# Kernel tuning notes

Hardware: AMD Instinct MI355X
Metric: run time of the kernel (lower is better)

## Reference

```python
import jax, jax.numpy as jnp
import numpy as np

B, L, D, NH, K, R = 2, 1024, 768, 12, 24, 768
HD = D // NH            # head_dim = 64
NFFT = 2048             # nearest power of two >= 2*L-1


def _spectral_filters():
    # Hankel matrix Z_{ij} = 2 / ((i+j)^3 - (i+j)), top-K eigvecs scaled by sigma^{1/4}
    e = np.arange(1, L + 1, dtype=np.float64)
    ipj = e[:, None] + e[None, :]
    Z = 2.0 / (ipj ** 3 - ipj)
    sigma, phi = np.linalg.eigh(Z)
    phi_k = phi[:, -K:] * (sigma[-K:] ** 0.25)
    return jnp.asarray(phi_k, dtype=jnp.float32)  # (L, K)


def setup_inputs() -> dict:
    key = jax.random.key(0)
    ks = jax.random.split(key, 16)
    s = 0.02
    lin = lambda k_, i, o: jax.random.normal(k_, (i, o), jnp.float32) * s
    return {
        "x": jax.random.normal(ks[0], (B, L, D), jnp.float32),
        "stu_filters": _spectral_filters(),
        "M_inputs": jax.random.normal(ks[1], (D, R), jnp.float32) * s,
        "M_filters": jax.random.normal(ks[2], (K, R), jnp.float32) * s,
        "wq_w": lin(ks[3], D, D), "wq_b": jnp.zeros((D,), jnp.float32),
        "wk_w": lin(ks[4], D, D), "wk_b": jnp.zeros((D,), jnp.float32),
        "wv_w": lin(ks[5], D, D), "wv_b": jnp.zeros((D,), jnp.float32),
        "wg_w": lin(ks[6], D, D), "wg_b": jnp.zeros((D,), jnp.float32),
        "wo_w": lin(ks[7], D, D), "wo_b": jnp.zeros((D,), jnp.float32),
    }


def _stu_features(x, stu_filters, M_inputs, M_filters):
    # tensordot STU path: project inputs and filters to rank R, then FFT causal conv
    u = x @ M_inputs                       # (B, L, R)
    phi = stu_filters @ M_filters          # (L, R)
    sgn = jnp.where(jnp.arange(L) % 2 == 0, 1.0, -1.0)[None, :, None]  # (1, L, 1)
    V = jnp.fft.rfft(phi, n=NFFT, axis=0)  # (NFFT//2+1, R)
    U = jnp.stack([u, u * sgn], axis=-1)   # (B, L, R, 2)
    Uf = jnp.fft.rfft(U, n=NFFT, axis=1)   # (B, NFFT//2+1, R, 2)
    conv = jnp.fft.irfft(V[None, :, :, None] * Uf, n=NFFT, axis=1)[:, :L]  # (B, L, R, 2)
    u_plus = conv[..., 0]
    u_minus = conv[..., 1] * sgn
    return u_plus + u_minus               # (B, L, R) with R == D


def reference(x, stu_filters, M_inputs, M_filters,
              wq_w, wq_b, wk_w, wk_b, wv_w, wv_b,
              wg_w, wg_b, wo_w, wo_b):
    x_tilde = _stu_features(x, stu_filters, M_inputs, M_filters)  # (B, L, D)

    heads = lambda y: y.reshape(B, L, NH, HD).transpose(0, 2, 1, 3)  # (B, H, L, h)
    q = heads(x @ wq_w + wq_b)
    k = heads(x @ wk_w + wk_b)
    v = heads(x @ wv_w + wv_b)

    # causal linear attention via cumulative outer-product state
    Z = jnp.einsum('bhtp,bhtn->bhtpn', v, k)     # (B, H, L, h, h)
    Hc = jnp.cumsum(Z, axis=2)
    Y = jnp.einsum('bhtp,bhtpn->bhtn', q, Hc)    # (B, H, L, h)
    y_attn = Y.transpose(0, 2, 1, 3).reshape(B, L, D)

    gate = jax.nn.sigmoid(x @ wg_w + wg_b)
    y = x_tilde + (y_attn - x_tilde) * gate
    return y @ wo_w + wo_b
```

## Files before the change

### kernel.cpp

```cpp
#include <hip/hip_runtime.h>
#include <math.h>

#define B_  2
#define L_  1024
#define D_  768
#define NH_ 12
#define HD_ 64
#define K_  24
#define R_  768
#define NC_ 16
#define CS_ 64

typedef __bf16 bf16x8 __attribute__((ext_vector_type(8)));
typedef float f32x4 __attribute__((ext_vector_type(4)));
typedef float f32x8 __attribute__((ext_vector_type(8)));
typedef unsigned short u16x8 __attribute__((ext_vector_type(8)));

__device__ inline unsigned short f2bf(float f) {
    union { float f; unsigned u; } v; v.f = f;
    unsigned r = v.u + 0x7FFFu + ((v.u >> 16) & 1u);
    return (unsigned short)(r >> 16);
}

__device__ inline ushort4 pack4(const f32x4 v) {
    ushort4 r;
    r.x = f2bf(v[0]); r.y = f2bf(v[1]); r.z = f2bf(v[2]); r.w = f2bf(v[3]);
    return r;
}

__device__ inline u16x8 pack8(const f32x8 v) {
    u16x8 r;
#pragma unroll
    for (int e = 0; e < 8; ++e) r[e] = f2bf(v[e]);
    return r;
}

__device__ inline f32x8 bf2f8(const u16x8 v) {
    f32x8 r;
#pragma unroll
    for (int e = 0; e < 8; ++e) {
        union { float f; unsigned u; } t;
        t.u = ((unsigned)v[e]) << 16;
        r[e] = t.f;
    }
    return r;
}

#define GLD_LDS16(g, l)                                                     \
    __builtin_amdgcn_global_load_lds(                                       \
        (const __attribute__((address_space(1))) void*)(g),                 \
        (__attribute__((address_space(3))) void*)(l), 16, 0, 0)

__global__ __launch_bounds__(256) void k_prep(const float* __restrict__ w0,
                                              const float* __restrict__ w1,
                                              const float* __restrict__ w2,
                                              const float* __restrict__ w3,
                                              const float* __restrict__ w4,
                                              const float* __restrict__ w5,
                                              unsigned short* __restrict__ Wt,
                                              const float* __restrict__ x,
                                              unsigned short* __restrict__ xb) {
    const int bid = blockIdx.x;
    const int tid = threadIdx.x;
    if (bid < 864) {
        const int z = bid / 144, rem = bid % 144;
        const float* W;
        switch (z) {
            case 0: W = w0; break;
            case 1: W = w1; break;
            case 2: W = w2; break;
            case 3: W = w3; break;
            case 4: W = w4; break;
            default: W = w5; break;
        }
        unsigned short* o = Wt + (size_t)z * D_ * D_;
        __shared__ float t[64][69];
        const int n0 = (rem % 12) * 64, k0 = (rem / 12) * 64;
        const int row = tid >> 4, c4 = (tid & 15) * 4;
#pragma unroll
        for (int i = 0; i < 4; ++i) {
            const float4 v = *reinterpret_cast<const float4*>(
                W + (size_t)(k0 + row + i * 16) * D_ + n0 + c4);
            t[row + i * 16][c4 + 0] = v.x;
            t[row + i * 16][c4 + 1] = v.y;
            t[row + i * 16][c4 + 2] = v.z;
            t[row + i * 16][c4 + 3] = v.w;
        }
        __syncthreads();
        const int orow = tid >> 4, oc4 = (tid & 15) * 4;
#pragma unroll
        for (int i = 0; i < 4; ++i) {
            const int nn = orow + i * 16;
            ushort4 o4;
            o4.x = f2bf(t[oc4 + 0][nn]);
            o4.y = f2bf(t[oc4 + 1][nn]);
            o4.z = f2bf(t[oc4 + 2][nn]);
            o4.w = f2bf(t[oc4 + 3][nn]);
            *reinterpret_cast<ushort4*>(o + (size_t)(n0 + nn) * D_ + k0 + oc4) = o4;
        }
    } else {
        const int i8 = ((bid - 864) * 256 + tid) * 8;
        float4 f0 = *reinterpret_cast<const float4*>(x + i8);
        float4 f1 = *reinterpret_cast<const float4*>(x + i8 + 4);
        u16x8 p;
        p[0] = f2bf(f0.x); p[1] = f2bf(f0.y); p[2] = f2bf(f0.z); p[3] = f2bf(f0.w);
        p[4] = f2bf(f1.x); p[5] = f2bf(f1.y); p[6] = f2bf(f1.z); p[7] = f2bf(f1.w);
        *reinterpret_cast<u16x8*>(xb + i8) = p;
    }
}

template <int FM, int FN>
__device__ __forceinline__ void gemm_core(const unsigned short* __restrict__ A,
                                          const unsigned short* __restrict__ Bt,
                                          const float* __restrict__ bias,
                                          int mode,
                                          float* __restrict__ cf,
                                          unsigned short* __restrict__ cbf,
                                          unsigned short* __restrict__ ct,
                                          int N, int Kd,
                                          int bm, int bn, int tid) {
    constexpr int BM = 2 * FM * 16;
    constexpr int BN = 2 * FN * 16;
    constexpr int CTS = BM + 4;
    __shared__ unsigned short smem[2 * BM * 64 + 2 * BN * 64];
    unsigned short (*As)[BM * 64] = (unsigned short (*)[BM * 64])smem;
    unsigned short (*Bs)[BN * 64] = (unsigned short (*)[BN * 64])(smem + 2 * BM * 64);
    const int lane = tid & 63, wave = tid >> 6;
    const int wm = (wave >> 1) * (FM * 16), wn = (wave & 1) * (FN * 16);
    const int l15 = lane & 15, lg = lane >> 4;

    f32x4 acc[FM][FN] = {};

    auto stage = [&](int buf, int k0) {
#pragma unroll
        for (int q = 0; q < FM; ++q) {
            const int s = q * 256 + tid;
            GLD_LDS16(A + (size_t)(bm + (s >> 3)) * Kd + k0 + (s & 7) * 8,
                      &As[buf][s * 8]);
        }
#pragma unroll
        for (int q = 0; q < FN; ++q) {
            const int s = q * 256 + tid;
            GLD_LDS16(Bt + (size_t)(bn + (s >> 3)) * Kd + k0 + (s & 7) * 8,
                      &Bs[buf][s * 8]);
        }
    };

    stage(0, 0);
    __syncthreads();
    int cur = 0;
    const int nt = Kd / 64;
    for (int t = 0; t < nt; ++t) {
        if (t + 1 < nt) stage(cur ^ 1, (t + 1) * 64);
#pragma unroll
        for (int ks = 0; ks < 2; ++ks) {
            const int kb = ks * 32 + lg * 8;
            bf16x8 a[FM], b[FN];
#pragma unroll
            for (int f = 0; f < FM; ++f)
                a[f] = *reinterpret_cast<const bf16x8*>(
                    &As[cur][(wm + f * 16 + l15) * 64 + kb]);
#pragma unroll
            for (int f = 0; f < FN; ++f)
                b[f] = *reinterpret_cast<const bf16x8*>(
                    &Bs[cur][(wn + f * 16 + l15) * 64 + kb]);
#pragma unroll
            for (int fm = 0; fm < FM; ++fm)
#pragma unroll
                for (int fn = 0; fn < FN; ++fn)
                    acc[fm][fn] = __builtin_amdgcn_mfma_f32_16x16x32_bf16(
                        a[fm], b[fn], acc[fm][fn], 0, 0, 0);
        }
        __syncthreads();
        cur ^= 1;
    }

#pragma unroll
    for (int fm = 0; fm < FM; ++fm)
#pragma unroll
        for (int fn = 0; fn < FN; ++fn) {
            const int cl = wn + fn * 16 + l15;
            const int col = bn + cl;
            const float bv = bias ? bias[col] : 0.f;
            const int rl = wm + fm * 16 + lg * 4;
            const int r0 = bm + rl;
            f32x4 v = acc[fm][fn];
            v[0] += bv; v[1] += bv; v[2] += bv; v[3] += bv;
            if (mode == 0) {
#pragma unroll
                for (int j = 0; j < 4; ++j)
                    cf[(size_t)(r0 + j) * N + col] = v[j];
            }
            if (mode & 1) {
#pragma unroll
                for (int j = 0; j < 4; ++j)
                    cbf[(size_t)(r0 + j) * D_ + col] = f2bf(v[j]);
            }
            if (mode & 2) {
                *reinterpret_cast<ushort4*>(&smem[cl * CTS + rl]) = pack4(v);
            }
        }

    if (mode & 2) {
        __syncthreads();
        const int bI = bm >> 10, l0 = bm & 1023;
#pragma unroll
        for (int q = 0; q < BN * BM / 8 / 256; ++q) {
            const int slot = q * 256 + tid;
            const int cl = slot / (BM / 8), seg = slot % (BM / 8);
            const int gcol = bn + cl;
            const int h = gcol >> 6, n = gcol & 63;
            *reinterpret_cast<u16x8*>(
                ct + (((size_t)bI * NH_ + h) * 64 + n) * (size_t)L_ + l0 + seg * 8) =
                *reinterpret_cast<const u16x8*>(&smem[cl * CTS + seg * 8]);
        }
    }
}

__global__ __launch_bounds__(256) void k_gemm(const unsigned short* __restrict__ A,
                                              const unsigned short* __restrict__ Bt,
                                              const float* __restrict__ bias,
                                              float* __restrict__ C,
                                              int N, int Kd) {
    gemm_core<1, 2>(A, Bt, bias, 0, C, nullptr, nullptr, N, Kd,
                    blockIdx.y * 32, blockIdx.x * 64, threadIdx.x);
}

__global__ __launch_bounds__(256) void k_gemm5(const unsigned short* __restrict__ A,
                                               const unsigned short* __restrict__ wt,
                                               const float* __restrict__ bq,
                                               const float* __restrict__ bk,
                                               const float* __restrict__ bv,
                                               const float* __restrict__ bg,
                                               unsigned short* __restrict__ ubf,
                                               unsigned short* __restrict__ qbf,
                                               unsigned short* __restrict__ ktb,
                                               unsigned short* __restrict__ vbf,
                                               unsigned short* __restrict__ vtb,
                                               unsigned short* __restrict__ gbf) {
    const int z = blockIdx.z;
    const float* bias = nullptr;
    int mode = 1;
    unsigned short* cbf = nullptr; unsigned short* ct = nullptr;
    switch (z) {
        case 0: mode = 1; cbf = ubf; bias = nullptr; break;
        case 1: mode = 1; cbf = qbf; bias = bq; break;
        case 2: mode = 2; ct = ktb; bias = bk; break;
        case 3: mode = 3; cbf = vbf; ct = vtb; bias = bv; break;
        default: mode = 1; cbf = gbf; bias = bg; break;
    }
    const unsigned short* Bt = wt + (size_t)z * D_ * D_;
    gemm_core<4, 4>(A, Bt, bias, mode, nullptr, cbf, ct, D_, D_,
                    blockIdx.y * 128, blockIdx.x * 128, threadIdx.x);
}

__global__ __launch_bounds__(256) void k_attn(const unsigned short* __restrict__ qbf,
                                              const unsigned short* __restrict__ vbf,
                                              const unsigned short* __restrict__ ktb,
                                              const unsigned short* __restrict__ vtb,
                                              unsigned short* __restrict__ yab,
                                              const float* __restrict__ F,
                                              const float* __restrict__ Mf,
                                              unsigned short* __restrict__ phiev) {
    const int tid = threadIdx.x;
    if (blockIdx.x >= 384) {
        const int idx = ((int)blockIdx.x - 384) * 256 + tid;
        const int r = idx % R_;
        const int n = idx / R_;
        float acc = 0.f;
#pragma unroll
        for (int kk = 0; kk < K_; ++kk)
            acc += F[(2 * n) * K_ + kk] * Mf[kk * R_ + r];
        phiev[idx] = f2bf(2.f * acc);
        return;
    }
    const int c = blockIdx.x & 15, h = (blockIdx.x >> 4) % NH_, b = blockIdx.x / (16 * NH_);
    __shared__ unsigned short Qs[64 * 64];
    __shared__ unsigned short Vs[64 * 64];
    __shared__ unsigned short Kc[64 * 64];
    __shared__ unsigned short Tk[2][64 * 64];
    __shared__ unsigned short Tv[2][64 * 64];
    __shared__ unsigned short Sl[64 * 72];
    __shared__ unsigned short Hl[64 * 72];

    const int lane = tid & 63, wave = tid >> 6;
    const int wr = (wave >> 1) * 32, wc = (wave & 1) * 32;
    const int l15 = lane & 15, lg = lane >> 4;

    {
        const size_t rowbase = ((size_t)(b * L_ + c * CS_)) * D_ + h * HD_;
        const size_t tbase = ((size_t)(b * NH_ + h)) * 64 * (size_t)L_ + c * 64;
#pragma unroll
        for (int q2 = 0; q2 < 2; ++q2) {
            const int s = q2 * 256 + tid;
            const int row = s >> 3, c8 = s & 7;
            GLD_LDS16(qbf + rowbase + (size_t)row * D_ + c8 * 8, &Qs[s * 8]);
            GLD_LDS16(vbf + rowbase + (size_t)row * D_ + c8 * 8, &Vs[s * 8]);
            GLD_LDS16(ktb + tbase + (size_t)row * L_ + c8 * 8, &Kc[s * 8]);
        }
    }

    auto stage_t = [&](int buf, int cc) {
        const size_t tb2 = ((size_t)(b * NH_ + h)) * 64 * (size_t)L_ + cc * 64;
#pragma unroll
        for (int q2 = 0; q2 < 2; ++q2) {
            const int s = q2 * 256 + tid;
            const int row = s >> 3, c8 = s & 7;
            GLD_LDS16(ktb + tb2 + (size_t)row * L_ + c8 * 8, &Tk[buf][s * 8]);
            GLD_LDS16(vtb + tb2 + (size_t)row * L_ + c8 * 8, &Tv[buf][s * 8]);
        }
    };

    if (c > 0) stage_t(0, 0);
    __syncthreads();

    f32x4 hacc[2][2] = {};
    int cur = 0;
    for (int cc = 0; cc < c; ++cc) {
        if (cc + 1 < c) stage_t(cur ^ 1, cc + 1);
#pragma unroll
        for (int ks = 0; ks < 2; ++ks) {
            const int kb = ks * 32 + lg * 8;
            bf16x8 av[2], bk[2];
#pragma unroll
            for (int f = 0; f < 2; ++f) {
                av[f] = *reinterpret_cast<const bf16x8*>(&Tv[cur][(wr + f * 16 + l15) * 64 + kb]);
                bk[f] = *reinterpret_cast<const bf16x8*>(&Tk[cur][(wc + f * 16 + l15) * 64 + kb]);
            }
#pragma unroll
            for (int fm = 0; fm < 2; ++fm)
#pragma unroll
                for (int fn = 0; fn < 2; ++fn)
                    hacc[fm][fn] = __builtin_amdgcn_mfma_f32_16x16x32_bf16(
                        av[fm], bk[fn], hacc[fm][fn], 0, 0, 0);
        }
        __syncthreads();
        cur ^= 1;
    }

    if (c > 0) {
#pragma unroll
        for (int fm = 0; fm < 2; ++fm)
#pragma unroll
            for (int fn = 0; fn < 2; ++fn) {
                const int n = wc + fn * 16 + l15;
                const int p0 = wr + fm * 16 + lg * 4;
                *reinterpret_cast<ushort4*>(&Hl[n * 72 + p0]) = pack4(hacc[fm][fn]);
            }
    }

    {
        f32x4 sacc[2][2] = {};
#pragma unroll
        for (int ks = 0; ks < 2; ++ks) {
            const int kb = ks * 32 + lg * 8;
            bf16x8 av[2], bq[2];
#pragma unroll
            for (int f = 0; f < 2; ++f) {
                av[f] = *reinterpret_cast<const bf16x8*>(&Vs[(wr + f * 16 + l15) * 64 + kb]);
                bq[f] = *reinterpret_cast<const bf16x8*>(&Qs[(wc + f * 16 + l15) * 64 + kb]);
            }
#pragma unroll
            for (int fm = 0; fm < 2; ++fm)
#pragma unroll
                for (int fn = 0; fn < 2; ++fn)
                    sacc[fm][fn] = __builtin_amdgcn_mfma_f32_16x16x32_bf16(
                        av[fm], bq[fn], sacc[fm][fn], 0, 0, 0);
        }
#pragma unroll
        for (int fm = 0; fm < 2; ++fm)
#pragma unroll
            for (int fn = 0; fn < 2; ++fn) {
                const int t = wc + fn * 16 + l15;
                const int s0 = wr + fm * 16 + lg * 4;
#pragma unroll
                for (int j = 0; j < 4; ++j)
                    if (s0 + j > t) sacc[fm][fn][j] = 0.f;
                *reinterpret_cast<ushort4*>(&Sl[t * 72 + s0]) = pack4(sacc[fm][fn]);
            }
    }
    __syncthreads();

    f32x4 yacc[2][2] = {};
#pragma unroll
    for (int ks = 0; ks < 2; ++ks) {
        const int kb = ks * 32 + lg * 8;
        bf16x8 ak[2], bs[2];
#pragma unroll
        for (int f = 0; f < 2; ++f) {
            ak[f] = *reinterpret_cast<const bf16x8*>(&Kc[(wr + f * 16 + l15) * 64 + kb]);
            bs[f] = *reinterpret_cast<const bf16x8*>(&Sl[(wc + f * 16 + l15) * 72 + kb]);
        }
#pragma unroll
        for (int fm = 0; fm < 2; ++fm)
#pragma unroll
            for (int fn = 0; fn < 2; ++fn)
                yacc[fm][fn] = __builtin_amdgcn_mfma_f32_16x16x32_bf16(
                    ak[fm], bs[fn], yacc[fm][fn], 0, 0, 0);
    }
    if (c > 0) {
#pragma unroll
        for (int ks = 0; ks < 2; ++ks) {
            const int kb = ks * 32 + lg * 8;
            bf16x8 ah[2], bq[2];
#pragma unroll
            for (int f = 0; f < 2; ++f) {
                ah[f] = *reinterpret_cast<const bf16x8*>(&Hl[(wr + f * 16 + l15) * 72 + kb]);
                bq[f] = *reinterpret_cast<const bf16x8*>(&Qs[(wc + f * 16 + l15) * 64 + kb]);
            }
#pragma unroll
            for (int fm = 0; fm < 2; ++fm)
#pragma unroll
                for (int fn = 0; fn < 2; ++fn)
                    yacc[fm][fn] = __builtin_amdgcn_mfma_f32_16x16x32_bf16(
                        ah[fm], bq[fn], yacc[fm][fn], 0, 0, 0);
        }
    }

#pragma unroll
    for (int fm = 0; fm < 2; ++fm)
#pragma unroll
        for (int fn = 0; fn < 2; ++fn) {
            const int n0 = wr + fm * 16 + lg * 4;
            const int t = wc + fn * 16 + l15;
            const size_t idx = ((size_t)(b * L_ + c * CS_ + t)) * D_ + h * HD_ + n0;
            *reinterpret_cast<ushort4*>(yab + idx) = pack4(yacc[fm][fn]);
        }
}

__global__ __launch_bounds__(768) void k_conv(const unsigned short* __restrict__ ubf,
                                              const unsigned short* __restrict__ phiev,
                                              const unsigned short* __restrict__ yab,
                                              const unsigned short* __restrict__ gbf,
                                              unsigned short* __restrict__ gx) {
    __shared__ u16x8 red[8][8][96];
    const int tid = threadIdx.x;
    const int g   = tid / 96;
    const int lr  = tid % 96;
    const int r   = lr * 8;
    const int m0  = blockIdx.x * 8;
    const int bp  = blockIdx.y;
    const int b   = bp >> 1, p = bp & 1;

    f32x8 acc[8] = {};
    f32x8 w[8]   = {};

    const int ns = g * 64;
    const int ne = min(ns + 64, m0 + 8);

    if (ns < ne) {
        if (g > 0) {
#pragma unroll
            for (int j = 1; j <= 7; ++j)
                w[(8 - j) & 7] = bf2f8(
                    *reinterpret_cast<const u16x8*>(phiev + (size_t)(ns - j) * R_ + r));
        }
        const unsigned short* pp = phiev + (size_t)ns * R_ + r;
        const unsigned short* up =
            ubf + ((size_t)(b * L_) + (size_t)(2 * (m0 + 7 - ns) + p)) * R_ + r;
        for (int i = ns; i < ne; i += 8) {
#pragma unroll
            for (int k = 0; k < 8; ++k) {
                const u16x8 pv = *reinterpret_cast<const u16x8*>(pp);
                const u16x8 uv = *reinterpret_cast<const u16x8*>(up);
                w[k] = bf2f8(pv);
                const f32x8 fu = bf2f8(uv);
#pragma unroll
                for (int a = 0; a < 8; ++a)
                    acc[a] += w[(k + a + 1) & 7] * fu;
                pp += R_;
                up -= 2 * R_;
            }
        }
    }

#pragma unroll
    for (int a = 0; a < 8; ++a) red[g][a][lr] = pack8(acc[a]);
    __syncthreads();

    const int a2 = tid / 96, l2 = tid % 96;
    f32x8 s = {};
#pragma unroll
    for (int g2 = 0; g2 < 8; ++g2) s += bf2f8(red[g2][a2][l2]);

    const size_t idx = ((size_t)(b * L_) + (size_t)(2 * (m0 + a2) + p)) * R_ + l2 * 8;
    const f32x8 yf = bf2f8(*reinterpret_cast<const u16x8*>(yab + idx));
    const f32x8 gf = bf2f8(*reinterpret_cast<const u16x8*>(gbf + idx));
    u16x8 o;
#pragma unroll
    for (int e = 0; e < 8; ++e) {
        const float sg = 1.f / (1.f + expf(-gf[e]));
        o[e] = f2bf(s[e] + (yf[e] - s[e]) * sg);
    }
    *reinterpret_cast<u16x8*>(gx + idx) = o;
}

extern "C" void kernel_launch(void* const* d_in, const int* in_sizes, int n_in,
                              void* d_out, int out_size, void* d_ws, size_t ws_size,
                              hipStream_t stream) {
    const float* x    = (const float*)d_in[0];
    const float* stu  = (const float*)d_in[1];
    const float* Mi   = (const float*)d_in[2];
    const float* Mf   = (const float*)d_in[3];
    const float* wq_w = (const float*)d_in[4];
    const float* wq_b = (const float*)d_in[5];
    const float* wk_w = (const float*)d_in[6];
    const float* wk_b = (const float*)d_in[7];
    const float* wv_w = (const float*)d_in[8];
    const float* wv_b = (const float*)d_in[9];
    const float* wg_w = (const float*)d_in[10];
    const float* wg_b = (const float*)d_in[11];
    const float* wo_w = (const float*)d_in[12];
    const float* wo_b = (const float*)d_in[13];
    float* out = (float*)d_out;

    char* ws = (char*)d_ws;
    size_t o = 0;
    const size_t WSZ = (size_t)D_ * D_;
    unsigned short* wbf   = (unsigned short*)(ws + o); o += 6 * WSZ * 2;
    unsigned short* xbf   = (unsigned short*)(ws + o); o += (size_t)B_ * L_ * D_ * 2;
    unsigned short* gx    = (unsigned short*)(ws + o); o += (size_t)B_ * L_ * D_ * 2;
    unsigned short* qbf   = (unsigned short*)(ws + o); o += (size_t)B_ * L_ * D_ * 2;
    unsigned short* vbf   = (unsigned short*)(ws + o); o += (size_t)B_ * L_ * D_ * 2;
    unsigned short* ubf   = (unsigned short*)(ws + o); o += (size_t)B_ * L_ * D_ * 2;
    unsigned short* gbf   = (unsigned short*)(ws + o); o += (size_t)B_ * L_ * D_ * 2;
    unsigned short* yab   = (unsigned short*)(ws + o); o += (size_t)B_ * L_ * D_ * 2;
    unsigned short* ktb   = (unsigned short*)(ws + o); o += (size_t)B_ * NH_ * 64 * L_ * 2;
    unsigned short* vtb   = (unsigned short*)(ws + o); o += (size_t)B_ * NH_ * 64 * L_ * 2;
    unsigned short* phiev = (unsigned short*)(ws + o); o += (size_t)(L_ / 2) * R_ * 2;

    unsigned short* wo_t = wbf + 5 * WSZ;

    const dim3 blk(256);

    k_prep<<<dim3(1632), blk, 0, stream>>>(Mi, wq_w, wk_w, wv_w, wg_w, wo_w, wbf,
                                           x, xbf);

    k_gemm5<<<dim3(D_ / 128, (B_ * L_) / 128, 5), blk, 0, stream>>>(
        xbf, wbf, wq_b, wk_b, wv_b, wg_b, ubf, qbf, ktb, vbf, vtb, gbf);

    k_attn<<<dim3(384 + 1536), blk, 0, stream>>>(qbf, vbf, ktb, vtb, yab,
                                                 stu, Mf, phiev);

    k_conv<<<dim3(L_ / 2 / 8, B_ * 2), dim3(768), 0, stream>>>(ubf, phiev, yab, gbf, gx);

    k_gemm<<<dim3(D_ / 64, (B_ * L_) / 32), blk, 0, stream>>>(gx, wo_t, wo_b, out, D_, D_);
}
```

Baseline: 91.94 us.

## Fuse five kernels into one persistent kernel with grid barriers

Replaces the five kernel launches (prep, fused QKVG GEMM, attention plus filter projection, convolution, output GEMM) with a single persistent kernel of 512 blocks. Stages are separated by atomic-counter grid barriers, and shared memory is one shared buffer carved up per stage. The conv stage is restructured to use 192 threads with 256-step chunks, and the output GEMM tile changes to 64x64. The aim is to remove launch gaps and tail effects between kernels. In exchange it risks deadlock if all 512 blocks are not co-resident, and it reduces parallelism within stages such as the conv and the final GEMM.

```diff
diff --git a/kernel.cpp b/kernel.cpp
--- a/kernel.cpp
+++ b/kernel.cpp
@@ -51,62 +51,18 @@
         (const __attribute__((address_space(1))) void*)(g),                 \
         (__attribute__((address_space(3))) void*)(l), 16, 0, 0)
 
-__global__ __launch_bounds__(256) void k_prep(const float* __restrict__ w0,
-                                              const float* __restrict__ w1,
-                                              const float* __restrict__ w2,
-                                              const float* __restrict__ w3,
-                                              const float* __restrict__ w4,
-                                              const float* __restrict__ w5,
-                                              unsigned short* __restrict__ Wt,
-                                              const float* __restrict__ x,
-                                              unsigned short* __restrict__ xb) {
-    const int bid = blockIdx.x;
-    const int tid = threadIdx.x;
-    if (bid < 864) {
-        const int z = bid / 144, rem = bid % 144;
-        const float* W;
-        switch (z) {
-            case 0: W = w0; break;
-            case 1: W = w1; break;
-            case 2: W = w2; break;
-            case 3: W = w3; break;
-            case 4: W = w4; break;
-            default: W = w5; break;
-        }
-        unsigned short* o = Wt + (size_t)z * D_ * D_;
-        __shared__ float t[64][69];
-        const int n0 = (rem % 12) * 64, k0 = (rem / 12) * 64;
-        const int row = tid >> 4, c4 = (tid & 15) * 4;
-#pragma unroll
-        for (int i = 0; i < 4; ++i) {
-            const float4 v = *reinterpret_cast<const float4*>(
-                W + (size_t)(k0 + row + i * 16) * D_ + n0 + c4);
-            t[row + i * 16][c4 + 0] = v.x;
-            t[row + i * 16][c4 + 1] = v.y;
-            t[row + i * 16][c4 + 2] = v.z;
-            t[row + i * 16][c4 + 3] = v.w;
-        }
-        __syncthreads();
-        const int orow = tid >> 4, oc4 = (tid & 15) * 4;
-#pragma unroll
-        for (int i = 0; i < 4; ++i) {
-            const int nn = orow + i * 16;
-            ushort4 o4;
-            o4.x = f2bf(t[oc4 + 0][nn]);
-            o4.y = f2bf(t[oc4 + 1][nn]);
-            o4.z = f2bf(t[oc4 + 2][nn]);
-            o4.w = f2bf(t[oc4 + 3][nn]);
-            *reinterpret_cast<ushort4*>(o + (size_t)(n0 + nn) * D_ + k0 + oc4) = o4;
-        }
-    } else {
-        const int i8 = ((bid - 864) * 256 + tid) * 8;
-        float4 f0 = *reinterpret_cast<const float4*>(x + i8);
-        float4 f1 = *reinterpret_cast<const float4*>(x + i8 + 4);
-        u16x8 p;
-        p[0] = f2bf(f0.x); p[1] = f2bf(f0.y); p[2] = f2bf(f0.z); p[3] = f2bf(f0.w);
-        p[4] = f2bf(f1.x); p[5] = f2bf(f1.y); p[6] = f2bf(f1.z); p[7] = f2bf(f1.w);
-        *reinterpret_cast<u16x8*>(xb + i8) = p;
-    }
+#define NBLK 512u
+
+__device__ inline void gridbar(unsigned* cnt) {
+    __syncthreads();
+    if (threadIdx.x == 0) {
+        __threadfence();
+        atomicAdd(cnt, 1u);
+        while (__hip_atomic_load(cnt, __ATOMIC_RELAXED,
+                                 __HIP_MEMORY_SCOPE_AGENT) < NBLK) {}
+        __threadfence();
+    }
+    __syncthreads();
 }
 
 template <int FM, int FN>
@@ -118,13 +74,15 @@
                                           unsigned short* __restrict__ cbf,
                                           unsigned short* __restrict__ ct,
                                           int N, int Kd,
-                                          int bm, int bn, int tid) {
+                                          int bm, int bn, int tid,
+                                          unsigned short* sm) {
     constexpr int BM = 2 * FM * 16;
     constexpr int BN = 2 * FN * 16;
     constexpr int CTS = BM + 4;
-    __shared__ unsigned short smem[2 * BM * 64 + 2 * BN * 64];
-    unsigned short (*As)[BM * 64] = (unsigned short (*)[BM * 64])smem;
-    unsigned short (*Bs)[BN * 64] = (unsigned short (*)[BN * 64])(smem + 2 * BM * 64);
+    unsigned short* As0 = sm;
+    unsigned short* As1 = sm + BM * 64;
+    unsigned short* Bs0 = sm + 2 * BM * 64;
+    unsigned short* Bs1 = sm + 2 * BM * 64 + BN * 64;
     const int lane = tid & 63, wave = tid >> 6;
     const int wm = (wave >> 1) * (FM * 16), wn = (wave & 1) * (FN * 16);
     const int l15 = lane & 15, lg = lane >> 4;
@@ -132,17 +90,19 @@
     f32x4 acc[FM][FN] = {};
 
     auto stage = [&](int buf, int k0) {
+        unsigned short* as = buf ? As1 : As0;
+        unsigned short* bs = buf ? Bs1 : Bs0;
 #pragma unroll
         for (int q = 0; q < FM; ++q) {
             const int s = q * 256 + tid;
             GLD_LDS16(A + (size_t)(bm + (s >> 3)) * Kd + k0 + (s & 7) * 8,
-                      &As[buf][s * 8]);
+                      &as[s * 8]);
         }
 #pragma unroll
         for (int q = 0; q < FN; ++q) {
             const int s = q * 256 + tid;
             GLD_LDS16(Bt + (size_t)(bn + (s >> 3)) * Kd + k0 + (s & 7) * 8,
-                      &Bs[buf][s * 8]);
+                      &bs[s * 8]);
         }
     };
 
@@ -152,18 +112,18 @@
     const int nt = Kd / 64;
     for (int t = 0; t < nt; ++t) {
         if (t + 1 < nt) stage(cur ^ 1, (t + 1) * 64);
+        const unsigned short* as = cur ? As1 : As0;
+        const unsigned short* bs = cur ? Bs1 : Bs0;
 #pragma unroll
         for (int ks = 0; ks < 2; ++ks) {
             const int kb = ks * 32 + lg * 8;
             bf16x8 a[FM], b[FN];
 #pragma unroll
             for (int f = 0; f < FM; ++f)
-                a[f] = *reinterpret_cast<const bf16x8*>(
-                    &As[cur][(wm + f * 16 + l15) * 64 + kb]);
+                a[f] = *reinterpret_cast<const bf16x8*>(&as[(wm + f * 16 + l15) * 64 + kb]);
 #pragma unroll
             for (int f = 0; f < FN; ++f)
-                b[f] = *reinterpret_cast<const bf16x8*>(
-                    &Bs[cur][(wn + f * 16 + l15) * 64 + kb]);
+                b[f] = *reinterpret_cast<const bf16x8*>(&bs[(wn + f * 16 + l15) * 64 + kb]);
 #pragma unroll
             for (int fm = 0; fm < FM; ++fm)
 #pragma unroll
@@ -197,7 +157,7 @@
                     cbf[(size_t)(r0 + j) * D_ + col] = f2bf(v[j]);
             }
             if (mode & 2) {
-                *reinterpret_cast<ushort4*>(&smem[cl * CTS + rl]) = pack4(v);
+                *reinterpret_cast<ushort4*>(&sm[cl * CTS + rl]) = pack4(v);
             }
         }
 
@@ -212,287 +172,345 @@
             const int h = gcol >> 6, n = gcol & 63;
             *reinterpret_cast<u16x8*>(
                 ct + (((size_t)bI * NH_ + h) * 64 + n) * (size_t)L_ + l0 + seg * 8) =
-                *reinterpret_cast<const u16x8*>(&smem[cl * CTS + seg * 8]);
-        }
-    }
-}
-
-__global__ __launch_bounds__(256) void k_gemm(const unsigned short* __restrict__ A,
-                                              const unsigned short* __restrict__ Bt,
-                                              const float* __restrict__ bias,
-                                              float* __restrict__ C,
-                                              int N, int Kd) {
-    gemm_core<1, 2>(A, Bt, bias, 0, C, nullptr, nullptr, N, Kd,
-                    blockIdx.y * 32, blockIdx.x * 64, threadIdx.x);
-}
-
-__global__ __launch_bounds__(256) void k_gemm5(const unsigned short* __restrict__ A,
-                                               const unsigned short* __restrict__ wt,
-                                               const float* __restrict__ bq,
-                                               const float* __restrict__ bk,
-                                               const float* __restrict__ bv,
-                                               const float* __restrict__ bg,
-                                               unsigned short* __restrict__ ubf,
-                                               unsigned short* __restrict__ qbf,
-                                               unsigned short* __restrict__ ktb,
-                                               unsigned short* __restrict__ vbf,
-                                               unsigned short* __restrict__ vtb,
-                                               unsigned short* __restrict__ gbf) {
-    const int z = blockIdx.z;
-    const float* bias = nullptr;
-    int mode = 1;
-    unsigned short* cbf = nullptr; unsigned short* ct = nullptr;
-    switch (z) {
-        case 0: mode = 1; cbf = ubf; bias = nullptr; break;
-        case 1: mode = 1; cbf = qbf; bias = bq; break;
-        case 2: mode = 2; ct = ktb; bias = bk; break;
-        case 3: mode = 3; cbf = vbf; ct = vtb; bias = bv; break;
-        default: mode = 1; cbf = gbf; bias = bg; break;
-    }
-    const unsigned short* Bt = wt + (size_t)z * D_ * D_;
-    gemm_core<4, 4>(A, Bt, bias, mode, nullptr, cbf, ct, D_, D_,
-                    blockIdx.y * 128, blockIdx.x * 128, threadIdx.x);
-}
-
-__global__ __launch_bounds__(256) void k_attn(const unsigned short* __restrict__ qbf,
-                                              const unsigned short* __restrict__ vbf,
-                                              const unsigned short* __restrict__ ktb,
-                                              const unsigned short* __restrict__ vtb,
-                                              unsigned short* __restrict__ yab,
-                                              const float* __restrict__ F,
-                                              const float* __restrict__ Mf,
-                                              unsigned short* __restrict__ phiev) {
+                *reinterpret_cast<const u16x8*>(&sm[cl * CTS + seg * 8]);
+        }
+    }
+}
+
+struct MegaArgs {
+    const float* x; const float* stu; const float* Mf;
+    const float* w0; const float* w1; const float* w2;
+    const float* w3; const float* w4; const float* w5;
+    const float* bq; const float* bk; const float* bv; const float* bg;
+    const float* bo;
+    unsigned short* wbf; unsigned short* xbf; unsigned short* gx;
+    unsigned short* qbf; unsigned short* vbf; unsigned short* ubf;
+    unsigned short* gbf; unsigned short* yab; unsigned short* ktb;
+    unsigned short* vtb; unsigned short* phiev;
+    float* out;
+    unsigned* bar;
+};
+
+#define SMEM_BYTES 75776
+
+__global__ __launch_bounds__(256, 2) void k_mono(MegaArgs A) {
+    __shared__ __align__(16) char smem_raw[SMEM_BYTES];
+    unsigned short* sm16 = (unsigned short*)smem_raw;
+    const int bid = blockIdx.x;
     const int tid = threadIdx.x;
-    if (blockIdx.x >= 384) {
-        const int idx = ((int)blockIdx.x - 384) * 256 + tid;
-        const int r = idx % R_;
-        const int n = idx / R_;
-        float acc = 0.f;
-#pragma unroll
-        for (int kk = 0; kk < K_; ++kk)
-            acc += F[(2 * n) * K_ + kk] * Mf[kk * R_ + r];
-        phiev[idx] = f2bf(2.f * acc);
-        return;
-    }
-    const int c = blockIdx.x & 15, h = (blockIdx.x >> 4) % NH_, b = blockIdx.x / (16 * NH_);
-    __shared__ unsigned short Qs[64 * 64];
-    __shared__ unsigned short Vs[64 * 64];
-    __shared__ unsigned short Kc[64 * 64];
-    __shared__ unsigned short Tk[2][64 * 64];
-    __shared__ unsigned short Tv[2][64 * 64];
-    __shared__ unsigned short Sl[64 * 72];
-    __shared__ unsigned short Hl[64 * 72];
-
-    const int lane = tid & 63, wave = tid >> 6;
-    const int wr = (wave >> 1) * 32, wc = (wave & 1) * 32;
-    const int l15 = lane & 15, lg = lane >> 4;
-
-    {
-        const size_t rowbase = ((size_t)(b * L_ + c * CS_)) * D_ + h * HD_;
-        const size_t tbase = ((size_t)(b * NH_ + h)) * 64 * (size_t)L_ + c * 64;
-#pragma unroll
-        for (int q2 = 0; q2 < 2; ++q2) {
-            const int s = q2 * 256 + tid;
-            const int row = s >> 3, c8 = s & 7;
-            GLD_LDS16(qbf + rowbase + (size_t)row * D_ + c8 * 8, &Qs[s * 8]);
-            GLD_LDS16(vbf + rowbase + (size_t)row * D_ + c8 * 8, &Vs[s * 8]);
-            GLD_LDS16(ktb + tbase + (size_t)row * L_ + c8 * 8, &Kc[s * 8]);
-        }
-    }
-
-    auto stage_t = [&](int buf, int cc) {
-        const size_t tb2 = ((size_t)(b * NH_ + h)) * 64 * (size_t)L_ + cc * 64;
-#pragma unroll
-        for (int q2 = 0; q2 < 2; ++q2) {
-            const int s = q2 * 256 + tid;
-            const int row = s >> 3, c8 = s & 7;
-            GLD_LDS16(ktb + tb2 + (size_t)row * L_ + c8 * 8, &Tk[buf][s * 8]);
-            GLD_LDS16(vtb + tb2 + (size_t)row * L_ + c8 * 8, &Tv[buf][s * 8]);
-        }
-    };
-
-    if (c > 0) stage_t(0, 0);
-    __syncthreads();
-
-    f32x4 hacc[2][2] = {};
-    int cur = 0;
-    for (int cc = 0; cc < c; ++cc) {
-        if (cc + 1 < c) stage_t(cur ^ 1, cc + 1);
+    const size_t WSZ = (size_t)D_ * D_;
+
+    for (int u = bid; u < 3168; u += NBLK) {
+        if (u < 864) {
+            const int z = u / 144, rem = u % 144;
+            const float* W;
+            switch (z) {
+                case 0: W = A.w0; break;
+                case 1: W = A.w1; break;
+                case 2: W = A.w2; break;
+                case 3: W = A.w3; break;
+                case 4: W = A.w4; break;
+                default: W = A.w5; break;
+            }
+            unsigned short* o = A.wbf + (size_t)z * WSZ;
+            float (*t)[69] = (float (*)[69])smem_raw;
+            const int n0 = (rem % 12) * 64, k0 = (rem / 12) * 64;
+            const int row = tid >> 4, c4 = (tid & 15) * 4;
+            __syncthreads();
+#pragma unroll
+            for (int i = 0; i < 4; ++i) {
+                const float4 v = *reinterpret_cast<const float4*>(
+                    W + (size_t)(k0 + row + i * 16) * D_ + n0 + c4);
+                t[row + i * 16][c4 + 0] = v.x;
+                t[row + i * 16][c4 + 1] = v.y;
+                t[row + i * 16][c4 + 2] = v.z;
+                t[row + i * 16][c4 + 3] = v.w;
+            }
+            __syncthreads();
+#pragma unroll
+            for (int i = 0; i < 4; ++i) {
+                const int nn = row + i * 16;
+                ushort4 o4;
+                o4.x = f2bf(t[c4 + 0][nn]);
+                o4.y = f2bf(t[c4 + 1][nn]);
+                o4.z = f2bf(t[c4 + 2][nn]);
+                o4.w = f2bf(t[c4 + 3][nn]);
+                *reinterpret_cast<ushort4*>(o + (size_t)(n0 + nn) * D_ + k0 + c4) = o4;
+            }
+        } else if (u < 1632) {
+            const int i8 = ((u - 864) * 256 + tid) * 8;
+            float4 f0 = *reinterpret_cast<const float4*>(A.x + i8);
+            float4 f1 = *reinterpret_cast<const float4*>(A.x + i8 + 4);
+            u16x8 p;
+            p[0] = f2bf(f0.x); p[1] = f2bf(f0.y); p[2] = f2bf(f0.z); p[3] = f2bf(f0.w);
+            p[4] = f2bf(f1.x); p[5] = f2bf(f1.y); p[6] = f2bf(f1.z); p[7] = f2bf(f1.w);
+            *reinterpret_cast<u16x8*>(A.xbf + i8) = p;
+        } else {
+            const int idx = (u - 1632) * 256 + tid;
+            const int r = idx % R_;
+            const int n = idx / R_;
+            float acc = 0.f;
+#pragma unroll
+            for (int kk = 0; kk < K_; ++kk)
+                acc += A.stu[(2 * n) * K_ + kk] * A.Mf[kk * R_ + r];
+            A.phiev[idx] = f2bf(2.f * acc);
+        }
+    }
+
+    gridbar(A.bar + 0);
+
+    if (bid < 480) {
+        const int z = bid / 96, rem = bid % 96;
+        const int bx = rem % 6, by = rem / 6;
+        const float* bias = nullptr;
+        int mode = 1;
+        unsigned short* cbf = nullptr; unsigned short* ct = nullptr;
+        switch (z) {
+            case 0: mode = 1; cbf = A.ubf; bias = nullptr; break;
+            case 1: mode = 1; cbf = A.qbf; bias = A.bq; break;
+            case 2: mode = 2; ct = A.ktb; bias = A.bk; break;
+            case 3: mode = 3; cbf = A.vbf; ct = A.vtb; bias = A.bv; break;
+            default: mode = 1; cbf = A.gbf; bias = A.bg; break;
+        }
+        gemm_core<4, 4>(A.xbf, A.wbf + (size_t)z * WSZ, bias, mode,
+                        nullptr, cbf, ct, D_, D_, by * 128, bx * 128, tid, sm16);
+    }
+
+    gridbar(A.bar + 1);
+
+    if (bid < 384) {
+        const int c = bid & 15, h = (bid >> 4) % NH_, b = bid / (16 * NH_);
+        unsigned short* Qs  = sm16;
+        unsigned short* Vs  = sm16 + 4096;
+        unsigned short* Kc  = sm16 + 8192;
+        unsigned short* Tk0 = sm16 + 12288;
+        unsigned short* Tk1 = sm16 + 16384;
+        unsigned short* Tv0 = sm16 + 20480;
+        unsigned short* Tv1 = sm16 + 24576;
+        unsigned short* Sl  = sm16 + 28672;
+        unsigned short* Hl  = sm16 + 33280;
+
+        const int lane = tid & 63, wave = tid >> 6;
+        const int wr = (wave >> 1) * 32, wc = (wave & 1) * 32;
+        const int l15 = lane & 15, lg = lane >> 4;
+
+        {
+            const size_t rowbase = ((size_t)(b * L_ + c * CS_)) * D_ + h * HD_;
+            const size_t tbase = ((size_t)(b * NH_ + h)) * 64 * (size_t)L_ + c * 64;
+#pragma unroll
+            for (int q2 = 0; q2 < 2; ++q2) {
+                const int s = q2 * 256 + tid;
+                const int row = s >> 3, c8 = s & 7;
+                GLD_LDS16(A.qbf + rowbase + (size_t)row * D_ + c8 * 8, &Qs[s * 8]);
+                GLD_LDS16(A.vbf + rowbase + (size_t)row * D_ + c8 * 8, &Vs[s * 8]);
+                GLD_LDS16(A.ktb + tbase + (size_t)row * L_ + c8 * 8, &Kc[s * 8]);
+            }
+        }
+
+        auto stage_t = [&](int buf, int cc) {
+            unsigned short* tk = buf ? Tk1 : Tk0;
+            unsigned short* tv = buf ? Tv1 : Tv0;
+            const size_t tb2 = ((size_t)(b * NH_ + h)) * 64 * (size_t)L_ + cc * 64;
+#pragma unroll
+            for (int q2 = 0; q2 < 2; ++q2) {
+                const int s = q2 * 256 + tid;
+                const int row = s >> 3, c8 = s & 7;
+                GLD_LDS16(A.ktb + tb2 + (size_t)row * L_ + c8 * 8, &tk[s * 8]);
+                GLD_LDS16(A.vtb + tb2 + (size_t)row * L_ + c8 * 8, &tv[s * 8]);
+            }
+        };
+
+        if (c > 0) stage_t(0, 0);
+        __syncthreads();
+
+        f32x4 hacc[2][2] = {};
+        int cur = 0;
+        for (int cc = 0; cc < c; ++cc) {
+            if (cc + 1 < c) stage_t(cur ^ 1, cc + 1);
+            const unsigned short* tk = cur ? Tk1 : Tk0;
+            const unsigned short* tv = cur ? Tv1 : Tv0;
+#pragma unroll
+            for (int ks = 0; ks < 2; ++ks) {
+                const int kb = ks * 32 + lg * 8;
+                bf16x8 av[2], bk[2];
+#pragma unroll
+                for (int f = 0; f < 2; ++f) {
+                    av[f] = *reinterpret_cast<const bf16x8*>(&tv[(wr + f * 16 + l15) * 64 + kb]);
+                    bk[f] = *reinterpret_cast<const bf16x8*>(&tk[(wc + f * 16 + l15) * 64 + kb]);
+                }
+#pragma unroll
+                for (int fm = 0; fm < 2; ++fm)
+#pragma unroll
+                    for (int fn = 0; fn < 2; ++fn)
+                        hacc[fm][fn] = __builtin_amdgcn_mfma_f32_16x16x32_bf16(
+                            av[fm], bk[fn], hacc[fm][fn], 0, 0, 0);
+            }
+            __syncthreads();
+            cur ^= 1;
+        }
+
+        if (c > 0) {
+#pragma unroll
+            for (int fm = 0; fm < 2; ++fm)
+#pragma unroll
+                for (int fn = 0; fn < 2; ++fn) {
+                    const int n = wc + fn * 16 + l15;
+                    const int p0 = wr + fm * 16 + lg * 4;
+                    *reinterpret_cast<ushort4*>(&Hl[n * 72 + p0]) = pack4(hacc[fm][fn]);
+                }
+        }
+
+        {
+            f32x4 sacc[2][2] = {};
+#pragma unroll
+            for (int ks = 0; ks < 2; ++ks) {
+                const int kb = ks * 32 + lg * 8;
+                bf16x8 av[2], bq[2];
+#pragma unroll
+                for (int f = 0; f < 2; ++f) {
+                    av[f] = *reinterpret_cast<const bf16x8*>(&Vs[(wr + f * 16 + l15) * 64 + kb]);
+                    bq[f] = *reinterpret_cast<const bf16x8*>(&Qs[(wc + f * 16 + l15) * 64 + kb]);
+                }
+#pragma unroll
+                for (int fm = 0; fm < 2; ++fm)
+#pragma unroll
+                    for (int fn = 0; fn < 2; ++fn)
+                        sacc[fm][fn] = __builtin_amdgcn_mfma_f32_16x16x32_bf16(
+                            av[fm], bq[fn], sacc[fm][fn], 0, 0, 0);
+            }
+#pragma unroll
+            for (int fm = 0; fm < 2; ++fm)
+#pragma unroll
+                for (int fn = 0; fn < 2; ++fn) {
+                    const int t = wc + fn * 16 + l15;
+                    const int s0 = wr + fm * 16 + lg * 4;
+#pragma unroll
+                    for (int j = 0; j < 4; ++j)
+                        if (s0 + j > t) sacc[fm][fn][j] = 0.f;
+                    *reinterpret_cast<ushort4*>(&Sl[t * 72 + s0]) = pack4(sacc[fm][fn]);
+                }
+        }
+        __syncthreads();
+
+        f32x4 yacc[2][2] = {};
 #pragma unroll
         for (int ks = 0; ks < 2; ++ks) {
             const int kb = ks * 32 + lg * 8;
-            bf16x8 av[2], bk[2];
+            bf16x8 ak[2], bs[2];
 #pragma unroll
             for (int f = 0; f < 2; ++f) {
-                av[f] = *reinterpret_cast<const bf16x8*>(&Tv[cur][(wr + f * 16 + l15) * 64 + kb]);
-                bk[f] = *reinterpret_cast<const bf16x8*>(&Tk[cur][(wc + f * 16 + l15) * 64 + kb]);
-            }
-#pragma unroll
-            for (int fm = 0; fm < 2; ++fm)
-#pragma unroll
-                for (int fn = 0; fn < 2; ++fn)
-                    hacc[fm][fn] = __builtin_amdgcn_mfma_f32_16x16x32_bf16(
-                        av[fm], bk[fn], hacc[fm][fn], 0, 0, 0);
-        }
-        __syncthreads();
-        cur ^= 1;
-    }
-
-    if (c > 0) {
-#pragma unroll
-        for (int fm = 0; fm < 2; ++fm)
-#pragma unroll
-            for (int fn = 0; fn < 2; ++fn) {
-                const int n = wc + fn * 16 + l15;
-                const int p0 = wr + fm * 16 + lg * 4;
-                *reinterpret_cast<ushort4*>(&Hl[n * 72 + p0]) = pack4(hacc[fm][fn]);
-            }
-    }
-
-    {
-        f32x4 sacc[2][2] = {};
-#pragma unroll
-        for (int ks = 0; ks < 2; ++ks) {
-            const int kb = ks * 32 + lg * 8;
-            bf16x8 av[2], bq[2];
-#pragma unroll
-            for (int f = 0; f < 2; ++f) {
-                av[f] = *reinterpret_cast<const bf16x8*>(&Vs[(wr + f * 16 + l15) * 64 + kb]);
-                bq[f] = *reinterpret_cast<const bf16x8*>(&Qs[(wc + f * 16 + l15) * 64 + kb]);
-            }
-#pragma unroll
-            for (int fm = 0; fm < 2; ++fm)
-#pragma unroll
-                for (int fn = 0; fn < 2; ++fn)
-                    sacc[fm][fn] = __builtin_amdgcn_mfma_f32_16x16x32_bf16(
-                        av[fm], bq[fn], sacc[fm][fn], 0, 0, 0);
-        }
-#pragma unroll
-        for (int fm = 0; fm < 2; ++fm)
-#pragma unroll
-            for (int fn = 0; fn < 2; ++fn) {
-                const int t = wc + fn * 16 + l15;
-                const int s0 = wr + fm * 16 + lg * 4;
-#pragma unroll
-                for (int j = 0; j < 4; ++j)
-                    if (s0 + j > t) sacc[fm][fn][j] = 0.f;
-                *reinterpret_cast<ushort4*>(&Sl[t * 72 + s0]) = pack4(sacc[fm][fn]);
-            }
-    }
-    __syncthreads();
-
-    f32x4 yacc[2][2] = {};
-#pragma unroll
-    for (int ks = 0; ks < 2; ++ks) {
-        const int kb = ks * 32 + lg * 8;
-        bf16x8 ak[2], bs[2];
-#pragma unroll
-        for (int f = 0; f < 2; ++f) {
-            ak[f] = *reinterpret_cast<const bf16x8*>(&Kc[(wr + f * 16 + l15) * 64 + kb]);
-            bs[f] = *reinterpret_cast<const bf16x8*>(&Sl[(wc + f * 16 + l15) * 72 + kb]);
-        }
-#pragma unroll
-        for (int fm = 0; fm < 2; ++fm)
-#pragma unroll
-            for (int fn = 0; fn < 2; ++fn)
-                yacc[fm][fn] = __builtin_amdgcn_mfma_f32_16x16x32_bf16(
-                    ak[fm], bs[fn], yacc[fm][fn], 0, 0, 0);
-    }
-    if (c > 0) {
-#pragma unroll
-        for (int ks = 0; ks < 2; ++ks) {
-            const int kb = ks * 32 + lg * 8;
-            bf16x8 ah[2], bq[2];
-#pragma unroll
-            for (int f = 0; f < 2; ++f) {
-                ah[f] = *reinterpret_cast<const bf16x8*>(&Hl[(wr + f * 16 + l15) * 72 + kb]);
-                bq[f] = *reinterpret_cast<const bf16x8*>(&Qs[(wc + f * 16 + l15) * 64 + kb]);
+                ak[f] = *reinterpret_cast<const bf16x8*>(&Kc[(wr + f * 16 + l15) * 64 + kb]);
+                bs[f] = *reinterpret_cast<const bf16x8*>(&Sl[(wc + f * 16 + l15) * 72 + kb]);
             }
 #pragma unroll
             for (int fm = 0; fm < 2; ++fm)
 #pragma unroll
                 for (int fn = 0; fn < 2; ++fn)
                     yacc[fm][fn] = __builtin_amdgcn_mfma_f32_16x16x32_bf16(
-                        ah[fm], bq[fn], yacc[fm][fn], 0, 0, 0);
-        }
-    }
-
-#pragma unroll
-    for (int fm = 0; fm < 2; ++fm)
-#pragma unroll
-        for (int fn = 0; fn < 2; ++fn) {
-            const int n0 = wr + fm * 16 + lg * 4;
-            const int t = wc + fn * 16 + l15;
-            const size_t idx = ((size_t)(b * L_ + c * CS_ + t)) * D_ + h * HD_ + n0;
-            *reinterpret_cast<ushort4*>(yab + idx) = pack4(yacc[fm][fn]);
-        }
-}
-
-__global__ __launch_bounds__(768) void k_conv(const unsigned short* __restrict__ ubf,
-                                              const unsigned short* __restrict__ phiev,
-                                              const unsigned short* __restrict__ yab,
-                                              const unsigned short* __restrict__ gbf,
-                                              unsigned short* __restrict__ gx) {
-    __shared__ u16x8 red[8][8][96];
-    const int tid = threadIdx.x;
-    const int g   = tid / 96;
-    const int lr  = tid % 96;
-    const int r   = lr * 8;
-    const int m0  = blockIdx.x * 8;
-    const int bp  = blockIdx.y;
-    const int b   = bp >> 1, p = bp & 1;
-
-    f32x8 acc[8] = {};
-    f32x8 w[8]   = {};
-
-    const int ns = g * 64;
-    const int ne = min(ns + 64, m0 + 8);
-
-    if (ns < ne) {
-        if (g > 0) {
-#pragma unroll
-            for (int j = 1; j <= 7; ++j)
-                w[(8 - j) & 7] = bf2f8(
-                    *reinterpret_cast<const u16x8*>(phiev + (size_t)(ns - j) * R_ + r));
-        }
-        const unsigned short* pp = phiev + (size_t)ns * R_ + r;
-        const unsigned short* up =
-            ubf + ((size_t)(b * L_) + (size_t)(2 * (m0 + 7 - ns) + p)) * R_ + r;
-        for (int i = ns; i < ne; i += 8) {
-#pragma unroll
-            for (int k = 0; k < 8; ++k) {
-                const u16x8 pv = *reinterpret_cast<const u16x8*>(pp);
-                const u16x8 uv = *reinterpret_cast<const u16x8*>(up);
-                w[k] = bf2f8(pv);
-                const f32x8 fu = bf2f8(uv);
-#pragma unroll
-                for (int a = 0; a < 8; ++a)
-                    acc[a] += w[(k + a + 1) & 7] * fu;
-                pp += R_;
-                up -= 2 * R_;
-            }
-        }
-    }
-
-#pragma unroll
-    for (int a = 0; a < 8; ++a) red[g][a][lr] = pack8(acc[a]);
-    __syncthreads();
-
-    const int a2 = tid / 96, l2 = tid % 96;
-    f32x8 s = {};
-#pragma unroll
-    for (int g2 = 0; g2 < 8; ++g2) s += bf2f8(red[g2][a2][l2]);
-
-    const size_t idx = ((size_t)(b * L_) + (size_t)(2 * (m0 + a2) + p)) * R_ + l2 * 8;
-    const f32x8 yf = bf2f8(*reinterpret_cast<const u16x8*>(yab + idx));
-    const f32x8 gf = bf2f8(*reinterpret_cast<const u16x8*>(gbf + idx));
-    u16x8 o;
-#pragma unroll
-    for (int e = 0; e < 8; ++e) {
-        const float sg = 1.f / (1.f + expf(-gf[e]));
-        o[e] = f2bf(s[e] + (yf[e] - s[e]) * sg);
-    }
-    *reinterpret_cast<u16x8*>(gx + idx) = o;
+                        ak[fm], bs[fn], yacc[fm][fn], 0, 0, 0);
+        }
+        if (c > 0) {
+#pragma unroll
+            for (int ks = 0; ks < 2; ++ks) {
+                const int kb = ks * 32 + lg * 8;
+                bf16x8 ah[2], bq[2];
+#pragma unroll
+                for (int f = 0; f < 2; ++f) {
+                    ah[f] = *reinterpret_cast<const bf16x8*>(&Hl[(wr + f * 16 + l15) * 72 + kb]);
+                    bq[f] = *reinterpret_cast<const bf16x8*>(&Qs[(wc + f * 16 + l15) * 64 + kb]);
+                }
+#pragma unroll
+                for (int fm = 0; fm < 2; ++fm)
+#pragma unroll
+                    for (int fn = 0; fn < 2; ++fn)
+                        yacc[fm][fn] = __builtin_amdgcn_mfma_f32_16x16x32_bf16(
+                            ah[fm], bq[fn], yacc[fm][fn], 0, 0, 0);
+            }
+        }
+
+#pragma unroll
+        for (int fm = 0; fm < 2; ++fm)
+#pragma unroll
+            for (int fn = 0; fn < 2; ++fn) {
+                const int n0 = wr + fm * 16 + lg * 4;
+                const int t = wc + fn * 16 + l15;
+                const size_t idx = ((size_t)(b * L_ + c * CS_ + t)) * D_ + h * HD_ + n0;
+                *reinterpret_cast<ushort4*>(A.yab + idx) = pack4(yacc[fm][fn]);
+            }
+    }
+
+    gridbar(A.bar + 2);
+
+    if (bid < 256) {
+        const int m0 = (bid & 63) * 8;
+        const int bp = bid >> 6;
+        const int b = bp >> 1, p = bp & 1;
+        u16x8* red = (u16x8*)sm16;
+
+        if (tid < 192) {
+            const int g = tid / 96, lr = tid % 96;
+            const int r = lr * 8;
+            f32x8 acc[8] = {};
+            f32x8 w[8] = {};
+            const int ns = g * 256;
+            const int ne = min(ns + 256, m0 + 8);
+            if (ns < ne) {
+                if (g > 0) {
+#pragma unroll
+                    for (int j = 1; j <= 7; ++j)
+                        w[(8 - j) & 7] = bf2f8(*reinterpret_cast<const u16x8*>(
+                            A.phiev + (size_t)(ns - j) * R_ + r));
+                }
+                const unsigned short* pp = A.phiev + (size_t)ns * R_ + r;
+                const unsigned short* up =
+                    A.ubf + ((size_t)(b * L_) + (size_t)(2 * (m0 + 7 - ns) + p)) * R_ + r;
+                for (int i = ns; i < ne; i += 8) {
+#pragma unroll
+                    for (int k = 0; k < 8; ++k) {
+                        const u16x8 pv = *reinterpret_cast<const u16x8*>(pp);
+                        const u16x8 uv = *reinterpret_cast<const u16x8*>(up);
+                        w[k] = bf2f8(pv);
+                        const f32x8 fu = bf2f8(uv);
+#pragma unroll
+                        for (int a = 0; a < 8; ++a)
+                            acc[a] += w[(k + a + 1) & 7] * fu;
+                        pp += R_;
+                        up -= 2 * R_;
+                    }
+                }
+            }
+#pragma unroll
+            for (int a = 0; a < 8; ++a) red[(g * 8 + a) * 96 + lr] = pack8(acc[a]);
+        }
+        __syncthreads();
+
+#pragma unroll
+        for (int q = 0; q < 3; ++q) {
+            const int slot = q * 256 + tid;
+            const int a2 = slot / 96, l2 = slot % 96;
+            f32x8 s = bf2f8(red[(0 * 8 + a2) * 96 + l2]) +
+                      bf2f8(red[(1 * 8 + a2) * 96 + l2]);
+            const size_t idx =
+                ((size_t)(b * L_) + (size_t)(2 * (m0 + a2) + p)) * R_ + l2 * 8;
+            const f32x8 yf = bf2f8(*reinterpret_cast<const u16x8*>(A.yab + idx));
+            const f32x8 gf = bf2f8(*reinterpret_cast<const u16x8*>(A.gbf + idx));
+            u16x8 o;
+#pragma unroll
+            for (int e = 0; e < 8; ++e) {
+                const float sg = 1.f / (1.f + expf(-gf[e]));
+                o[e] = f2bf(s[e] + (yf[e] - s[e]) * sg);
+            }
+            *reinterpret_cast<u16x8*>(A.gx + idx) = o;
+        }
+    }
+
+    gridbar(A.bar + 3);
+
+    if (bid < 384) {
+        const int bx = bid % 12, by = bid / 12;
+        gemm_core<2, 2>(A.gx, A.wbf + 5 * WSZ, A.bo, 0, A.out, nullptr, nullptr,
+                        D_, D_, by * 64, bx * 64, tid, sm16);
+    }
 }
 
 extern "C" void kernel_launch(void* const* d_in, const int* in_sizes, int n_in,
@@ -516,6 +534,7 @@
 
     char* ws = (char*)d_ws;
     size_t o = 0;
+    unsigned* bar = (unsigned*)(ws + o); o += 256;
     const size_t WSZ = (size_t)D_ * D_;
     unsigned short* wbf   = (unsigned short*)(ws + o); o += 6 * WSZ * 2;
     unsigned short* xbf   = (unsigned short*)(ws + o); o += (size_t)B_ * L_ * D_ * 2;
@@ -529,20 +548,19 @@
     unsigned short* vtb   = (unsigned short*)(ws + o); o += (size_t)B_ * NH_ * 64 * L_ * 2;
     unsigned short* phiev = (unsigned short*)(ws + o); o += (size_t)(L_ / 2) * R_ * 2;
 
-    unsigned short* wo_t = wbf + 5 * WSZ;
-
-    const dim3 blk(256);
-
-    k_prep<<<dim3(1632), blk, 0, stream>>>(Mi, wq_w, wk_w, wv_w, wg_w, wo_w, wbf,
-                                           x, xbf);
-
-    k_gemm5<<<dim3(D_ / 128, (B_ * L_) / 128, 5), blk, 0, stream>>>(
-        xbf, wbf, wq_b, wk_b, wv_b, wg_b, ubf, qbf, ktb, vbf, vtb, gbf);
-
-    k_attn<<<dim3(384 + 1536), blk, 0, stream>>>(qbf, vbf, ktb, vtb, yab,
-                                                 stu, Mf, phiev);
-
-    k_conv<<<dim3(L_ / 2 / 8, B_ * 2), dim3(768), 0, stream>>>(ubf, phiev, yab, gbf, gx);
-
-    k_gemm<<<dim3(D_ / 64, (B_ * L_) / 32), blk, 0, stream>>>(gx, wo_t, wo_b, out, D_, D_);
-}
+    MegaArgs margs;
+    margs.x = x; margs.stu = stu; margs.Mf = Mf;
+    margs.w0 = Mi; margs.w1 = wq_w; margs.w2 = wk_w;
+    margs.w3 = wv_w; margs.w4 = wg_w; margs.w5 = wo_w;
+    margs.bq = wq_b; margs.bk = wk_b; margs.bv = wv_b; margs.bg = wg_b;
+    margs.bo = wo_b;
+    margs.wbf = wbf; margs.xbf = xbf; margs.gx = gx;
+    margs.qbf = qbf; margs.vbf = vbf; margs.ubf = ubf;
+    margs.gbf = gbf; margs.yab = yab; margs.ktb = ktb;
+    margs.vtb = vtb; margs.phiev = phiev;
+    margs.out = out;
+    margs.bar = bar;
+
+    hipMemsetAsync(bar, 0, 256, stream);
+    k_mono<<<dim3(NBLK), dim3(256), 0, stream>>>(margs);
+}
```

Measured after the change: 311.8 us. 239% more time.
